# Optimization experiments

Measured on AMD Instinct MI355X. Metric: run time of the kernel, lower is better.

Reference implementation:

```python
import jax, jax.numpy as jnp
import numpy as np

N_SAMPLES = 32768
WS, STEP = 2048, 256
DILATIONS = (1, 2, 4, 8, 16, 32, 64, 1)
N_KEEP = 16
N_ROOMS = 8
N_ATOMS = 2048


def stft_mag(x):
    # x: (B, 1, N) -> magnitude spectrogram (B, 128, 1025)
    B = x.shape[0]
    xx = jnp.pad(x.reshape(B, -1), ((0, 0), (0, WS - STEP)))  # right-pad -> exactly N/STEP frames
    n_frames = N_SAMPLES // STEP  # 128
    idx = jnp.arange(n_frames)[:, None] * STEP + jnp.arange(WS)[None, :]
    frames = xx[:, idx] * jnp.hanning(WS)[None, None, :]  # (B, 128, 2048)
    return jnp.abs(jnp.fft.rfft(frames, axis=-1))


def fft_convolve(a, b):
    # linear convolution via zero-padding to 2N, sliced back to N
    n = a.shape[-1]
    pad = [(0, 0)] * (a.ndim - 1) + [(0, n)]
    sa = jnp.fft.rfft(jnp.pad(a, pad), axis=-1)
    sb = jnp.fft.rfft(jnp.pad(b, pad), axis=-1)
    return jnp.fft.irfft(sa * sb, n=2 * n, axis=-1)[..., :n]


def mlp(z, w, b, g, be, ow, ob):
    # LinearOutputStack: (Linear -> LayerNorm -> leaky_relu) x3 -> Linear
    for i in range(w.shape[0]):
        z = z @ w[i] + b[i]
        mu = jnp.mean(z, -1, keepdims=True)
        var = jnp.var(z, -1, keepdims=True)
        z = (z - mu) / jnp.sqrt(var + 1e-5) * g[i] + be[i]
        z = jax.nn.leaky_relu(z, 0.2)
    return z @ ow + ob


def setup_inputs() -> dict:
    key = jax.random.key(0)
    ks = jax.random.split(key, 12)
    s = 0.02
    B = 4
    decay = jnp.linspace(1.0, 0.0, N_SAMPLES) ** 2
    atoms = jax.random.uniform(ks[0], (N_ATOMS, N_SAMPLES), minval=-0.01, maxval=0.01) * decay[None, :]
    imp = jax.random.normal(ks[1], (N_ROOMS, N_SAMPLES)) * (jnp.linspace(1.0, 0.0, N_SAMPLES) ** 4)[None, :]
    imp = imp / jnp.linalg.norm(imp, axis=-1, keepdims=True)
    return {
        'x': jax.random.normal(ks[2], (B, 1, N_SAMPLES)),
        'atoms': atoms,
        'enc_w': jax.random.normal(ks[3], (8, 1024, 1024, 2)) * s,
        'enc_b': jnp.zeros((8, 1024)),
        'up_w': jax.random.normal(ks[4], (256, 1024)) * s,
        'up_b': jnp.zeros((256,)),
        'lat_w': jax.random.normal(ks[5], (1024, 16)) * s,
        'lat_b': jnp.zeros((16,)),
        'room_w': jax.random.normal(ks[6], (3, 16, 16)) * s,
        'room_b': jnp.zeros((3, 16)),
        'room_g': jnp.ones((3, 16)),
        'room_be': jnp.zeros((3, 16)),
        'room_ow': jax.random.normal(ks[7], (16, N_ROOMS)) * s,
        'room_ob': jnp.zeros((N_ROOMS,)),
        'mix_w': jax.random.normal(ks[8], (3, 16, 16)) * s,
        'mix_b': jnp.zeros((3, 16)),
        'mix_g': jnp.ones((3, 16)),
        'mix_be': jnp.zeros((3, 16)),
        'mix_ow': jax.random.normal(ks[9], (16, 1)) * s,
        'mix_ob': jnp.zeros((1,)),
        'impulses': imp,
    }


def reference(x, atoms, enc_w, enc_b, up_w, up_b, lat_w, lat_b,
              room_w, room_b, room_g, room_be, room_ow, room_ob,
              mix_w, mix_b, mix_g, mix_be, mix_ow, mix_ob, impulses):
    B = x.shape[0]
    # ---- encode ----
    spec = stft_mag(x)[..., :1024]                    # (B, 128, 1024)
    h = jnp.transpose(spec, (0, 2, 1))                # (B, 1024, 128)
    for i, d in enumerate(DILATIONS):                  # anti-causal dilated residual stack
        y = jnp.pad(h, ((0, 0), (0, 0), (0, d)))      # pad the FUTURE
        y = jax.lax.conv_general_dilated(y, enc_w[i], (1,), 'VALID', rhs_dilation=(d,),
                                         dimension_numbers=('NCH', 'OIH', 'NCH'))
        h = h + jax.nn.leaky_relu(y + enc_b[i][None, :, None], 0.2)
    z = jnp.mean(h, axis=-1)                          # (B, 1024)
    dense = z @ lat_w + lat_b                          # (B, 16)
    dense = dense / (jnp.linalg.norm(dense, axis=-1, keepdims=True) + 1e-8)  # unit_norm
    # ---- generate ----
    enc = jnp.einsum('bct,oc->bot', h, up_w) + up_b[None, :, None]  # 1x1 conv -> (B, 256, 128)
    full = jnp.zeros((B, 256, N_SAMPLES), enc.dtype).at[:, :, ::STEP].set(enc)
    # sparsify2: flattened top-k over (channel, time)
    flat = full.reshape(B, -1)
    vals, idx = jax.lax.top_k(flat, N_KEEP)           # (B, 16)
    ch = idx // N_SAMPLES                              # atom/channel index per event
    t = idx % N_SAMPLES                                # time index per event
    packed = jnp.zeros((B, N_KEEP, N_SAMPLES), full.dtype).at[
        jnp.arange(B)[:, None], jnp.arange(N_KEEP)[None, :], t].set(vals)
    subset = atoms[ch]                                 # gather -> (B, 16, 32768)
    events = fft_convolve(packed, subset)              # (B, 16, N)
    dry = jnp.sum(events, axis=1, keepdims=True)       # (B, 1, N)
    # ---- reverb ----
    room = jax.nn.softmax(mlp(dense, room_w, room_b, room_g, room_be, room_ow, room_ob), axis=-1)
    impulse = room @ impulses                          # (B, N)
    wet = fft_convolve(dry, impulse[:, None, :])
    mix = jax.nn.sigmoid(mlp(dense, mix_w, mix_b, mix_g, mix_be, mix_ow, mix_ob))[:, :, None]  # (B,1,1)
    return dry * mix + wet * (1.0 - mix)
```

## Files before the change

### kernel.cpp

```cpp
#include <hip/hip_runtime.h>
#include <hip/hip_bf16.h>
#include <math.h>

#define NSMP 32768
#define NFR 128
#define NCH 1024
#define NB 4

typedef __attribute__((ext_vector_type(8))) short short8;
typedef __attribute__((ext_vector_type(4))) float f32x4;
typedef unsigned short ushort;

__device__ __forceinline__ void split_bf(float v, ushort& h, ushort& l) {
  __hip_bfloat16 bh = __float2bfloat16(v);
  float r = v - __bfloat162float(bh);
  __hip_bfloat16 bl = __float2bfloat16(r);
  h = *reinterpret_cast<ushort*>(&bh);
  l = *reinterpret_cast<ushort*>(&bl);
}

__device__ __forceinline__ void gload_lds16(const ushort* g, ushort* l) {
  __builtin_amdgcn_global_load_lds((const __attribute__((address_space(1))) void*)g,
                                   (__attribute__((address_space(3))) void*)l, 16, 0, 0);
}

__global__ __launch_bounds__(256) void stft_kernel(const float* __restrict__ x,
                                                   float* __restrict__ h,
                                                   ushort* __restrict__ hTh,
                                                   ushort* __restrict__ hTl) {
  __shared__ float re[2048];
  __shared__ float im[2048];
  __shared__ float twr[1024];
  __shared__ float twi[1024];
  int bid = blockIdx.x;
  int b = bid >> 7;
  int f = bid & 127;
  int tid = threadIdx.x;
  const float TWO_PI = 6.28318530717958647692f;
  for (int k = tid; k < 1024; k += 256) {
    float ang = -TWO_PI * (float)k / 2048.0f;
    float sn, cs;
    sincosf(ang, &sn, &cs);
    twr[k] = cs; twi[k] = sn;
  }
  for (int i = tid; i < 2048; i += 256) {
    int rev = (int)(__brev((unsigned)i) >> 21);
    int pos = f * 256 + rev;
    float v = (pos < NSMP) ? x[b * NSMP + pos] : 0.f;
    float w = 0.5f - 0.5f * cosf(TWO_PI * (float)rev / 2047.0f);
    re[i] = v * w;
    im[i] = 0.f;
  }
  __syncthreads();
  for (int s = 0; s < 11; ++s) {
    for (int q = 0; q < 4; ++q) {
      int bi = tid + q * 256;
      int half = 1 << s;
      int j = bi & (half - 1);
      int i0 = ((bi >> s) << (s + 1)) | j;
      int i1 = i0 + half;
      int ti = j << (10 - s);
      float cs = twr[ti], sn = twi[ti];
      float ur = re[i0], ui = im[i0];
      float vr = re[i1], vi = im[i1];
      float tr = vr * cs - vi * sn;
      float tti = vr * sn + vi * cs;
      re[i0] = ur + tr; im[i0] = ui + tti;
      re[i1] = ur - tr; im[i1] = ui - tti;
    }
    __syncthreads();
  }
  for (int k = tid; k < 1024; k += 256) {
    float m = sqrtf(re[k] * re[k] + im[k] * im[k]);
    h[(b * NCH + k) * NFR + f] = m;
    ushort hi, lo;
    split_bf(m, hi, lo);
    size_t tidx = ((size_t)b * 192 + f) * 1024 + k;
    hTh[tidx] = hi;
    hTl[tidx] = lo;
  }
}

__global__ void zeropad_kernel(ushort* p0, ushort* p1, ushort* p2, ushort* p3) {
  int row = 128 + blockIdx.x;
  int b = blockIdx.y;
  size_t idx = ((size_t)b * 192 + row) * 1024 + threadIdx.x * 4;
  uint2 z = {0u, 0u};
  *(uint2*)&p0[idx] = z;
  *(uint2*)&p1[idx] = z;
  *(uint2*)&p2[idx] = z;
  *(uint2*)&p3[idx] = z;
}

__global__ __launch_bounds__(256) void wsplit_kernel(const float* __restrict__ encw,
                                                     ushort* __restrict__ w0h, ushort* __restrict__ w0l,
                                                     ushort* __restrict__ w1h, ushort* __restrict__ w1l) {
  size_t F = (size_t)blockIdx.x * 256 + threadIdx.x;
  float4 v = ((const float4*)encw)[F];
  size_t lo_idx = F >> 9;
  int c0 = (int)(F & 511) * 2;
  size_t base = lo_idx * 1024 + c0;
  ushort h0, l0, h1, l1;
  split_bf(v.x, h0, l0);
  split_bf(v.z, h1, l1);
  *(ushort2*)&w0h[base] = (ushort2){h0, h1};
  *(ushort2*)&w0l[base] = (ushort2){l0, l1};
  split_bf(v.y, h0, l0);
  split_bf(v.w, h1, l1);
  *(ushort2*)&w1h[base] = (ushort2){h0, h1};
  *(ushort2*)&w1l[base] = (ushort2){l0, l1};
}

__global__ __launch_bounds__(256) void conv_mfma(const ushort* __restrict__ hTh,
                                                 const ushort* __restrict__ hTl,
                                                 const ushort* __restrict__ w0h, const ushort* __restrict__ w0l,
                                                 const ushort* __restrict__ w1h, const ushort* __restrict__ w1l,
                                                 int D, float* __restrict__ yp) {
  __shared__ ushort lds[24576];
  int tid = threadIdx.x;
  int og = blockIdx.x * 64;
  int b = blockIdx.y;
  int s = blockIdx.z;
  int wid = tid >> 6, lane = tid & 63;
  int wr = (wid >> 1) * 32, wc = (wid & 1) * 64;
  int lr = lane & 15, lk = lane >> 4;
  int srow = lane >> 2;
  int scol = ((lane & 3) ^ ((lane >> 3) & 3)) * 8;

  f32x4 acc[2][4];
#pragma unroll
  for (int m = 0; m < 2; ++m)
#pragma unroll
    for (int n = 0; n < 4; ++n) acc[m][n] = (f32x4){0.f, 0.f, 0.f, 0.f};

  const ushort* hb_h = hTh + (size_t)b * 192 * 1024;
  const ushort* hb_l = hTl + (size_t)b * 192 * 1024;

  auto stage = [&](int buf, int p) {
    const ushort* Wh = (p < 4) ? w0h : w1h;
    const ushort* Wl = (p < 4) ? w0l : w1l;
    int rowoff = (p < 4) ? 0 : D;
    int c0 = s * 128 + (p & 3) * 32 + scol;
    ushort* base = &lds[buf * 12288];
    int ra = og + wid * 16 + srow;
    gload_lds16(Wh + (size_t)ra * 1024 + c0, base + wid * 512);
    gload_lds16(Wl + (size_t)ra * 1024 + c0, base + 2048 + wid * 512);
    int rb0 = rowoff + wid * 32 + srow;
    int rb1 = rb0 + 16;
    gload_lds16(hb_h + (size_t)rb0 * 1024 + c0, base + 4096 + wid * 1024);
    gload_lds16(hb_h + (size_t)rb1 * 1024 + c0, base + 4096 + wid * 1024 + 512);
    gload_lds16(hb_l + (size_t)rb0 * 1024 + c0, base + 8192 + wid * 1024);
    gload_lds16(hb_l + (size_t)rb1 * 1024 + c0, base + 8192 + wid * 1024 + 512);
  };

  auto compute = [&](int buf) {
    const ushort* base = &lds[buf * 12288];
    short8 ah[2], al[2], bh[4], bl[4];
#pragma unroll
    for (int m = 0; m < 2; ++m) {
      int ar = wr + m * 16 + lr;
      int off = ar * 32 + ((lk ^ ((ar >> 1) & 3)) << 3);
      ah[m] = *(const short8*)&base[off];
      al[m] = *(const short8*)&base[2048 + off];
    }
#pragma unroll
    for (int n = 0; n < 4; ++n) {
      int br = wc + n * 16 + lr;
      int off = br * 32 + ((lk ^ ((br >> 1) & 3)) << 3);
      bh[n] = *(const short8*)&base[4096 + off];
      bl[n] = *(const short8*)&base[8192 + off];
    }
#pragma unroll
    for (int m = 0; m < 2; ++m)
#pragma unroll
      for (int n = 0; n < 4; ++n) {
        acc[m][n] = __builtin_amdgcn_mfma_f32_16x16x32_bf16(ah[m], bh[n], acc[m][n], 0, 0, 0);
        acc[m][n] = __builtin_amdgcn_mfma_f32_16x16x32_bf16(ah[m], bl[n], acc[m][n], 0, 0, 0);
        acc[m][n] = __builtin_amdgcn_mfma_f32_16x16x32_bf16(al[m], bh[n], acc[m][n], 0, 0, 0);
      }
  };

  stage(0, 0);
  asm volatile("s_waitcnt vmcnt(0)" ::: "memory");
  __syncthreads();
#pragma unroll 2
  for (int p = 0; p < 8; ++p) {
    if (p < 7) stage((p + 1) & 1, p + 1);
    compute(p & 1);
    asm volatile("s_waitcnt vmcnt(0)" ::: "memory");
    __syncthreads();
  }

  float* dst = yp + (size_t)(s * 4 + b) * 131072;
#pragma unroll
  for (int m = 0; m < 2; ++m)
#pragma unroll
    for (int n = 0; n < 4; ++n)
#pragma unroll
      for (int r = 0; r < 4; ++r) {
        int orow = og + wr + m * 16 + lk * 4 + r;
        int col = wc + n * 16 + lr;
        dst[orow * 128 + col] = acc[m][n][r];
      }
}

__global__ __launch_bounds__(256) void conv_epi(const float* __restrict__ yp,
                                                const float* __restrict__ hin,
                                                const float* __restrict__ bias,
                                                float* __restrict__ hout,
                                                ushort* __restrict__ hTh,
                                                ushort* __restrict__ hTl) {
  __shared__ float T[16][132];
  int og = blockIdx.x * 16;
  int b = blockIdx.y;
  int tid = threadIdx.x;
#pragma unroll
  for (int j = 0; j < 8; ++j) {
    int flat = j * 256 + tid;
    int o = flat >> 7, t = flat & 127;
    size_t base = ((size_t)b * NCH + og + o) * NFR + t;
    float v = 0.f;
#pragma unroll
    for (int sl = 0; sl < 8; ++sl) v += yp[(size_t)sl * 524288 + base];
    v += bias[og + o];
    v = (v > 0.f) ? v : 0.2f * v;
    float r = hin[base] + v;
    hout[base] = r;
    T[o][t] = r;
  }
  __syncthreads();
#pragma unroll
  for (int j = 0; j < 8; ++j) {
    int flat = j * 256 + tid;
    int t = flat >> 4, o = flat & 15;
    ushort hi, lo;
    split_bf(T[o][t], hi, lo);
    size_t tidx = ((size_t)b * 192 + t) * 1024 + og + o;
    hTh[tidx] = hi;
    hTl[tidx] = lo;
  }
}

template <int TAPS, int D, int KTOT, int SPLIT, int MROWS>
__global__ __launch_bounds__(256, 2) void gemm_f32(const float* __restrict__ hin,
                                                   const float* __restrict__ W,
                                                   float* __restrict__ yp) {
  __shared__ float As[64][68];
  __shared__ float Bs[64][132];
  int tid = threadIdx.x;
  int og = blockIdx.x * 64;
  int b = blockIdx.y;
  int s = blockIdx.z;
  const float* hb = hin + (size_t)b * (NCH * NFR);
  int tx = tid & 15;
  int ty = tid >> 4;
  float acc[4][8] = {};
  const int KS = KTOT / SPLIT;
  for (int kt = 0; kt < KS / 64; ++kt) {
    int k0 = s * KS + kt * 64;
    __syncthreads();
    {
      int r = tid >> 2;
      int seg = (tid & 3) * 16;
      const float4* src = (const float4*)(W + (size_t)(og + r) * KTOT + k0 + seg);
#pragma unroll
      for (int q = 0; q < 4; ++q) {
        float4 v = src[q];
        int row = seg + 4 * q;
#pragma unroll
        for (int i = 0; i < 4; ++i) {
          int rr = row + i;
          int col = r ^ (((rr >> 4) & 1) << 2);
          float val = (i == 0) ? v.x : (i == 1) ? v.y : (i == 2) ? v.z : v.w;
          As[rr][col] = val;
        }
      }
    }
    {
      int r = tid >> 2;
      int tq = (tid & 3) * 32;
      int c = k0 + r;
      const float4* src = (const float4*)(hb + (size_t)c * NFR + tq);
#pragma unroll
      for (int q = 0; q < 8; ++q) *(float4*)&Bs[r][tq + 4 * q] = src[q];
    }
    __syncthreads();
#pragma unroll 8
    for (int kk = 0; kk < 64; ++kk) {
      int ca = (ty * 4) ^ (((kk >> 4) & 1) << 2);
      float4 a0 = *(const float4*)&As[kk][ca];
      float4 b0 = *(const float4*)&Bs[kk][tx * 4];
      float4 b1 = *(const float4*)&Bs[kk][tx * 4 + 64];
      float av[4] = {a0.x, a0.y, a0.z, a0.w};
      float bv[8] = {b0.x, b0.y, b0.z, b0.w, b1.x, b1.y, b1.z, b1.w};
#pragma unroll
      for (int i = 0; i < 4; ++i)
#pragma unroll
        for (int j = 0; j < 8; ++j)
          acc[i][j] += av[i] * bv[j];
    }
  }
  float* ypb = yp + (size_t)s * (NB * MROWS * NFR) + (size_t)b * MROWS * NFR;
#pragma unroll
  for (int i = 0; i < 4; ++i) {
    int o = og + ty * 4 + i;
    *(float4*)&ypb[o * NFR + tx * 4] = (float4){acc[i][0], acc[i][1], acc[i][2], acc[i][3]};
    *(float4*)&ypb[o * NFR + tx * 4 + 64] = (float4){acc[i][4], acc[i][5], acc[i][6], acc[i][7]};
  }
}

__global__ __launch_bounds__(256) void dense_mlp_kernel(
    const float* __restrict__ h,
    const float* __restrict__ latw, const float* __restrict__ latb,
    const float* __restrict__ rw, const float* __restrict__ rb,
    const float* __restrict__ rg, const float* __restrict__ rbe,
    const float* __restrict__ rowt, const float* __restrict__ rob,
    const float* __restrict__ mw, const float* __restrict__ mb,
    const float* __restrict__ mg, const float* __restrict__ mbe,
    const float* __restrict__ mow, const float* __restrict__ mob,
    float* __restrict__ room, float* __restrict__ mixv) {
  __shared__ float z[1024];
  int b = blockIdx.x;
  int tid = threadIdx.x;
  const float* hb = h + b * NCH * NFR;
  for (int c = tid; c < 1024; c += 256) {
    float s = 0.f;
    const float* r = hb + c * NFR;
#pragma unroll 8
    for (int t = 0; t < NFR; ++t) s += r[t];
    z[c] = s * (1.f / 128.f);
  }
  __syncthreads();
  if (tid >= 64) return;
  int j = tid & 15;
  int p = tid >> 4;
  float dsum = 0.f;
  for (int c = p * 256; c < p * 256 + 256; ++c)
    dsum += z[c] * latw[c * 16 + j];
  dsum += __shfl_xor(dsum, 16);
  dsum += __shfl_xor(dsum, 32);
  float dj = dsum + latb[j];
  float sq = dj * dj;
  sq += __shfl_xor(sq, 1, 16);
  sq += __shfl_xor(sq, 2, 16);
  sq += __shfl_xor(sq, 4, 16);
  sq += __shfl_xor(sq, 8, 16);
  float a = dj / (sqrtf(sq) + 1e-8f);

  const float* W = rw;  const float* Bb = rb;
  const float* G = rg;  const float* Be = rbe;
  for (int which = 0; which < 2; ++which) {
    float v = a;
    for (int l = 0; l < 3; ++l) {
      float accv = Bb[l * 16 + j];
      for (int k = 0; k < 16; ++k) {
        float ak = __shfl(v, (tid & 48) | k);
        accv += ak * W[(l * 16 + k) * 16 + j];
      }
      float mu = accv;
      mu += __shfl_xor(mu, 1, 16); mu += __shfl_xor(mu, 2, 16);
      mu += __shfl_xor(mu, 4, 16); mu += __shfl_xor(mu, 8, 16);
      mu *= (1.f / 16.f);
      float dv = accv - mu;
      float var = dv * dv;
      var += __shfl_xor(var, 1, 16); var += __shfl_xor(var, 2, 16);
      var += __shfl_xor(var, 4, 16); var += __shfl_xor(var, 8, 16);
      var *= (1.f / 16.f);
      float xn = dv * rsqrtf(var + 1e-5f) * G[l * 16 + j] + Be[l * 16 + j];
      v = (xn > 0.f) ? xn : 0.2f * xn;
    }
    if (which == 0) {
      int r = tid & 7;
      float logit = rob[r];
      for (int k = 0; k < 16; ++k) {
        float ak = __shfl(v, (tid & 48) | k);
        logit += ak * rowt[k * 8 + r];
      }
      float mx = logit;
      mx = fmaxf(mx, __shfl_xor(mx, 1, 8));
      mx = fmaxf(mx, __shfl_xor(mx, 2, 8));
      mx = fmaxf(mx, __shfl_xor(mx, 4, 8));
      float e = expf(logit - mx);
      float se = e;
      se += __shfl_xor(se, 1, 8);
      se += __shfl_xor(se, 2, 8);
      se += __shfl_xor(se, 4, 8);
      if (tid < 8) room[b * 8 + r] = e / se;
      W = mw; Bb = mb; G = mg; Be = mbe;
    } else {
      float logit = mob[0];
      for (int k = 0; k < 16; ++k) {
        float ak = __shfl(v, (tid & 48) | k);
        logit += ak * mow[k];
      }
      if (tid == 0) mixv[b] = 1.f / (1.f + expf(-logit));
    }
  }
}

__global__ __launch_bounds__(256) void topk_kernel(const float* __restrict__ ep,
                                                   const float* __restrict__ upb,
                                                   float* __restrict__ vals,
                                                   int* __restrict__ chs,
                                                   int* __restrict__ tps) {
  __shared__ float swv[4];
  __shared__ int swi[4];
  int b = blockIdx.x;
  int tid = threadIdx.x;
  const float* e = ep + b * 32768;
  float lv[16];
  int li[16];
#pragma unroll
  for (int q = 0; q < 16; ++q) { lv[q] = -INFINITY; li[q] = 0x7fffffff; }
  for (int i = tid; i < 32768; i += 256) {
    float v = e[i] + e[131072 + i] + e[262144 + i] + e[393216 + i] + upb[i >> 7];
    if (v > lv[15]) {
      float cv = v; int ci = i;
#pragma unroll
      for (int q = 0; q < 16; ++q) {
        if (cv > lv[q]) {
          float tv = lv[q]; int ti = li[q];
          lv[q] = cv; li[q] = ci;
          cv = tv; ci = ti;
        }
      }
    }
  }
  for (int round = 0; round < 16; ++round) {
    float cv = lv[0];
    int ci = li[0];
#pragma unroll
    for (int off = 1; off < 64; off <<= 1) {
      float ov = __shfl_xor(cv, off);
      int oi = __shfl_xor(ci, off);
      if (ov > cv || (ov == cv && oi < ci)) { cv = ov; ci = oi; }
    }
    if ((tid & 63) == 0) { swv[tid >> 6] = cv; swi[tid >> 6] = ci; }
    __syncthreads();
    float wv = swv[0]; int wi = swi[0];
#pragma unroll
    for (int w = 1; w < 4; ++w) {
      float v2 = swv[w]; int i2 = swi[w];
      if (v2 > wv || (v2 == wv && i2 < wi)) { wv = v2; wi = i2; }
    }
    if (tid == 0) {
      vals[b * 16 + round] = (wv > 0.f) ? wv : 0.f;
      chs[b * 16 + round] = wi >> 7;
      tps[b * 16 + round] = (wi & 127) * 256;
    }
    if (li[0] == wi) {
#pragma unroll
      for (int q = 0; q < 15; ++q) { lv[q] = lv[q + 1]; li[q] = li[q + 1]; }
      lv[15] = -INFINITY; li[15] = 0x7fffffff;
    }
    __syncthreads();
  }
}

__global__ void dry_kernel(const float* __restrict__ atoms,
                           const float* __restrict__ vals, const int* __restrict__ chs,
                           const int* __restrict__ tps, float* __restrict__ dry) {
  int b = blockIdx.y;
  int n = blockIdx.x * 256 + threadIdx.x;
  float acc = 0.f;
#pragma unroll 4
  for (int j = 0; j < 16; ++j) {
    float v = vals[b * 16 + j];
    int tp = tps[b * 16 + j];
    int ch = chs[b * 16 + j];
    if (v != 0.f && n >= tp)
      acc += v * atoms[(size_t)ch * NSMP + (n - tp)];
  }
  dry[b * NSMP + n] = acc;
}

__global__ void impulse_kernel(const float* __restrict__ imps,
                               const float* __restrict__ room, float* __restrict__ imp) {
  int b = blockIdx.y;
  int n = blockIdx.x * 256 + threadIdx.x;
  float acc = 0.f;
#pragma unroll
  for (int r = 0; r < 8; ++r)
    acc += room[b * 8 + r] * imps[r * NSMP + n];
  imp[b * NSMP + n] = acc;
}

#define IS(a) is[(a) + ((a) >> 5)]
__global__ __launch_bounds__(256) void wet_kernel(const float* __restrict__ dry,
                                                  const float* __restrict__ impulse,
                                                  float* __restrict__ wp) {
  int s = blockIdx.x;
  int nt = blockIdx.y;
  int b = blockIdx.z;
  if (s > nt) return;
  __shared__ float is[4224];
  __shared__ float dsr[2048];
  int tid = threadIdx.x;
  int n0 = nt * 2048;
  int m0 = s * 2048;
  int base = n0 - m0 - 2047;
  const float* impb = impulse + b * NSMP;
  for (int k = tid; k < 4096; k += 256) {
    int idx = base + k;
    IS(k) = (idx >= 0 && idx < NSMP) ? impb[idx] : 0.f;
  }
  for (int i = tid; i < 2048; i += 256)
    dsr[i] = dry[b * NSMP + m0 + 2047 - i];
  __syncthreads();
  int aw = tid * 8;
  float w[8];
#pragma unroll
  for (int j = 0; j < 8; ++j) w[j] = IS(aw + j);
  float acc[8] = {};
  for (int jb = 0; jb < 2048; jb += 8) {
    float4 d0 = *(const float4*)&dsr[jb];
    float4 d1 = *(const float4*)&dsr[jb + 4];
    float dv[8] = {d0.x, d0.y, d0.z, d0.w, d1.x, d1.y, d1.z, d1.w};
#pragma unroll
    for (int e = 0; e < 8; ++e) {
      float dval = dv[e];
#pragma unroll
      for (int i = 0; i < 8; ++i)
        acc[i] += dval * w[(e + i) & 7];
      w[e] = IS(aw + jb + e + 8);
    }
  }
  float* dst = wp + (size_t)s * (NB * NSMP) + (size_t)b * NSMP + n0 + aw;
  *(float4*)dst = (float4){acc[0], acc[1], acc[2], acc[3]};
  *(float4*)(dst + 4) = (float4){acc[4], acc[5], acc[6], acc[7]};
}

__global__ void out_kernel(const float* __restrict__ dry, const float* __restrict__ wp,
                           const float* __restrict__ mixv, float* __restrict__ out) {
  int b = blockIdx.y;
  int n = blockIdx.x * 256 + threadIdx.x;
  float m = mixv[b];
  float wv = 0.f;
  int smax = n >> 11;
  for (int s = 0; s <= smax; ++s)
    wv += wp[(size_t)s * (NB * NSMP) + b * NSMP + n];
  out[b * NSMP + n] = dry[b * NSMP + n] * m + wv * (1.f - m);
}

extern "C" void kernel_launch(void* const* d_in, const int* in_sizes, int n_in,
                              void* d_out, int out_size, void* d_ws, size_t ws_size,
                              hipStream_t stream) {
  const float* x    = (const float*)d_in[0];
  const float* atoms= (const float*)d_in[1];
  const float* encw = (const float*)d_in[2];
  const float* encb = (const float*)d_in[3];
  const float* upw  = (const float*)d_in[4];
  const float* upb  = (const float*)d_in[5];
  const float* latw = (const float*)d_in[6];
  const float* latb = (const float*)d_in[7];
  const float* rw   = (const float*)d_in[8];
  const float* rb   = (const float*)d_in[9];
  const float* rg   = (const float*)d_in[10];
  const float* rbe  = (const float*)d_in[11];
  const float* rowt = (const float*)d_in[12];
  const float* rob  = (const float*)d_in[13];
  const float* mw   = (const float*)d_in[14];
  const float* mb   = (const float*)d_in[15];
  const float* mg   = (const float*)d_in[16];
  const float* mbe  = (const float*)d_in[17];
  const float* mow  = (const float*)d_in[18];
  const float* mob  = (const float*)d_in[19];
  const float* imps = (const float*)d_in[20];

  float* f    = (float*)d_ws;
  float* h0   = f;
  float* h1   = f + 524288;
  float* yp   = f + 1048576;
  float* ep   = yp;
  float* wp   = yp + 524288;
  float* dry  = f + 5242880;
  float* imp  = f + 5373952;
  float* room = f + 5636096;
  float* mixv = f + 5636128;
  float* vals = f + 5636160;
  int*   chs  = (int*)(f + 5636224);
  int*   tps  = (int*)(f + 5636288);
  ushort* w0h  = (ushort*)(f + 6000000);
  ushort* w0l  = w0h + 8388608;
  ushort* w1h  = w0l + 8388608;
  ushort* w1l  = w1h + 8388608;
  ushort* hTh0 = w1l + 8388608;
  ushort* hTl0 = hTh0 + 786432;
  ushort* hTh1 = hTl0 + 786432;
  ushort* hTl1 = hTh1 + 786432;

  wsplit_kernel<<<16384, 256, 0, stream>>>(encw, w0h, w0l, w1h, w1l);
  zeropad_kernel<<<dim3(64, 4), 256, 0, stream>>>(hTh0, hTl0, hTh1, hTl1);
  stft_kernel<<<512, 256, 0, stream>>>(x, h0, hTh0, hTl0);

  float* bufs[2] = {h0, h1};
  ushort* hThb[2] = {hTh0, hTh1};
  ushort* hTlb[2] = {hTl0, hTl1};
  const int dil[8] = {1, 2, 4, 8, 16, 32, 64, 1};
  for (int l = 0; l < 8; ++l) {
    int pi = l & 1, po = (l + 1) & 1;
    conv_mfma<<<dim3(16, 4, 8), 256, 0, stream>>>(
        hThb[pi], hTlb[pi],
        w0h + (size_t)l * 1048576, w0l + (size_t)l * 1048576,
        w1h + (size_t)l * 1048576, w1l + (size_t)l * 1048576,
        dil[l], yp);
    conv_epi<<<dim3(64, 4), 256, 0, stream>>>(yp, bufs[pi], encb + l * 1024,
                                              bufs[po], hThb[po], hTlb[po]);
  }

  dense_mlp_kernel<<<4, 256, 0, stream>>>(h0, latw, latb, rw, rb, rg, rbe, rowt, rob,
                                          mw, mb, mg, mbe, mow, mob, room, mixv);
  gemm_f32<1, 0, 1024, 4, 256><<<dim3(4, 4, 4), 256, 0, stream>>>(h0, upw, ep);
  topk_kernel<<<4, 256, 0, stream>>>(ep, upb, vals, chs, tps);
  dry_kernel<<<dim3(128, 4), 256, 0, stream>>>(atoms, vals, chs, tps, dry);
  impulse_kernel<<<dim3(128, 4), 256, 0, stream>>>(imps, room, imp);
  wet_kernel<<<dim3(16, 16, 4), 256, 0, stream>>>(dry, imp, wp);
  out_kernel<<<dim3(128, 4), 256, 0, stream>>>(dry, wp, mixv, (float*)d_out);
}
```

Measured before the change: 522.7 us.

## Enlarge conv MFMA tile, triple-buffer staging, fuse small kernels, split gemm K

The dilated-conv MFMA kernel now computes a 128x128 output tile per block instead of 64x128. It uses three LDS buffers with a prefetch depth of two, and each wave loads one operand plane. The zero-pad kernel is folded into the STFT kernel, and the dry and impulse kernels are merged into one launch. The up-projection gemm is split over 16 K-slices, which topk sums. These changes aim to raise data reuse and cut launch overhead, at the cost of fewer conv blocks (less parallelism), more LDS per block and more partial-sum traffic.

```diff
diff --git a/kernel.cpp b/kernel.cpp
--- a/kernel.cpp
+++ b/kernel.cpp
@@ -27,7 +27,9 @@
 __global__ __launch_bounds__(256) void stft_kernel(const float* __restrict__ x,
                                                    float* __restrict__ h,
                                                    ushort* __restrict__ hTh,
-                                                   ushort* __restrict__ hTl) {
+                                                   ushort* __restrict__ hTl,
+                                                   ushort* __restrict__ hTh1,
+                                                   ushort* __restrict__ hTl1) {
   __shared__ float re[2048];
   __shared__ float im[2048];
   __shared__ float twr[1024];
@@ -37,6 +39,12 @@
   int f = bid & 127;
   int tid = threadIdx.x;
   const float TWO_PI = 6.28318530717958647692f;
+  if (f < 64) {
+    size_t pidx = ((size_t)b * 192 + 128 + f) * 1024 + tid * 4;
+    uint2 z = {0u, 0u};
+    *(uint2*)&hTh[pidx] = z;  *(uint2*)&hTl[pidx] = z;
+    *(uint2*)&hTh1[pidx] = z; *(uint2*)&hTl1[pidx] = z;
+  }
   for (int k = tid; k < 1024; k += 256) {
     float ang = -TWO_PI * (float)k / 2048.0f;
     float sn, cs;
@@ -79,17 +87,6 @@
     hTh[tidx] = hi;
     hTl[tidx] = lo;
   }
-}
-
-__global__ void zeropad_kernel(ushort* p0, ushort* p1, ushort* p2, ushort* p3) {
-  int row = 128 + blockIdx.x;
-  int b = blockIdx.y;
-  size_t idx = ((size_t)b * 192 + row) * 1024 + threadIdx.x * 4;
-  uint2 z = {0u, 0u};
-  *(uint2*)&p0[idx] = z;
-  *(uint2*)&p1[idx] = z;
-  *(uint2*)&p2[idx] = z;
-  *(uint2*)&p3[idx] = z;
 }
 
 __global__ __launch_bounds__(256) void wsplit_kernel(const float* __restrict__ encw,
@@ -116,20 +113,20 @@
                                                  const ushort* __restrict__ w0h, const ushort* __restrict__ w0l,
                                                  const ushort* __restrict__ w1h, const ushort* __restrict__ w1l,
                                                  int D, float* __restrict__ yp) {
-  __shared__ ushort lds[24576];
+  __shared__ ushort lds[49152];
   int tid = threadIdx.x;
-  int og = blockIdx.x * 64;
+  int og = blockIdx.x * 128;
   int b = blockIdx.y;
   int s = blockIdx.z;
   int wid = tid >> 6, lane = tid & 63;
-  int wr = (wid >> 1) * 32, wc = (wid & 1) * 64;
+  int wr = (wid >> 1) * 64, wc = (wid & 1) * 64;
   int lr = lane & 15, lk = lane >> 4;
   int srow = lane >> 2;
-  int scol = ((lane & 3) ^ ((lane >> 3) & 3)) * 8;
-
-  f32x4 acc[2][4];
-#pragma unroll
-  for (int m = 0; m < 2; ++m)
+  int sgr = ((lane & 3) ^ ((lane >> 3) & 3)) * 8;
+
+  f32x4 acc[4][4];
+#pragma unroll
+  for (int m = 0; m < 4; ++m)
 #pragma unroll
     for (int n = 0; n < 4; ++n) acc[m][n] = (f32x4){0.f, 0.f, 0.f, 0.f};
 
@@ -140,38 +137,39 @@
     const ushort* Wh = (p < 4) ? w0h : w1h;
     const ushort* Wl = (p < 4) ? w0l : w1l;
     int rowoff = (p < 4) ? 0 : D;
-    int c0 = s * 128 + (p & 3) * 32 + scol;
-    ushort* base = &lds[buf * 12288];
-    int ra = og + wid * 16 + srow;
-    gload_lds16(Wh + (size_t)ra * 1024 + c0, base + wid * 512);
-    gload_lds16(Wl + (size_t)ra * 1024 + c0, base + 2048 + wid * 512);
-    int rb0 = rowoff + wid * 32 + srow;
-    int rb1 = rb0 + 16;
-    gload_lds16(hb_h + (size_t)rb0 * 1024 + c0, base + 4096 + wid * 1024);
-    gload_lds16(hb_h + (size_t)rb1 * 1024 + c0, base + 4096 + wid * 1024 + 512);
-    gload_lds16(hb_l + (size_t)rb0 * 1024 + c0, base + 8192 + wid * 1024);
-    gload_lds16(hb_l + (size_t)rb1 * 1024 + c0, base + 8192 + wid * 1024 + 512);
+    int c0 = s * 128 + (p & 3) * 32 + sgr;
+    ushort* dbase = &lds[buf * 16384 + wid * 4096];
+#pragma unroll
+    for (int j = 0; j < 8; ++j) {
+      int row = j * 16 + srow;
+      const ushort* src;
+      if (wid == 0)      src = Wh   + (size_t)(og + row) * 1024 + c0;
+      else if (wid == 1) src = Wl   + (size_t)(og + row) * 1024 + c0;
+      else if (wid == 2) src = hb_h + (size_t)(rowoff + row) * 1024 + c0;
+      else               src = hb_l + (size_t)(rowoff + row) * 1024 + c0;
+      gload_lds16(src, dbase + j * 512);
+    }
   };
 
   auto compute = [&](int buf) {
-    const ushort* base = &lds[buf * 12288];
-    short8 ah[2], al[2], bh[4], bl[4];
-#pragma unroll
-    for (int m = 0; m < 2; ++m) {
+    const ushort* base = &lds[buf * 16384];
+    short8 ah[4], al[4], bh[4], bl[4];
+#pragma unroll
+    for (int m = 0; m < 4; ++m) {
       int ar = wr + m * 16 + lr;
       int off = ar * 32 + ((lk ^ ((ar >> 1) & 3)) << 3);
       ah[m] = *(const short8*)&base[off];
-      al[m] = *(const short8*)&base[2048 + off];
+      al[m] = *(const short8*)&base[4096 + off];
     }
 #pragma unroll
     for (int n = 0; n < 4; ++n) {
       int br = wc + n * 16 + lr;
       int off = br * 32 + ((lk ^ ((br >> 1) & 3)) << 3);
-      bh[n] = *(const short8*)&base[4096 + off];
-      bl[n] = *(const short8*)&base[8192 + off];
-    }
-#pragma unroll
-    for (int m = 0; m < 2; ++m)
+      bh[n] = *(const short8*)&base[8192 + off];
+      bl[n] = *(const short8*)&base[12288 + off];
+    }
+#pragma unroll
+    for (int m = 0; m < 4; ++m)
 #pragma unroll
       for (int n = 0; n < 4; ++n) {
         acc[m][n] = __builtin_amdgcn_mfma_f32_16x16x32_bf16(ah[m], bh[n], acc[m][n], 0, 0, 0);
@@ -181,19 +179,19 @@
   };
 
   stage(0, 0);
-  asm volatile("s_waitcnt vmcnt(0)" ::: "memory");
-  __syncthreads();
-#pragma unroll 2
+  stage(1, 1);
+#pragma unroll
   for (int p = 0; p < 8; ++p) {
-    if (p < 7) stage((p + 1) & 1, p + 1);
-    compute(p & 1);
-    asm volatile("s_waitcnt vmcnt(0)" ::: "memory");
-    __syncthreads();
+    if (p < 7) asm volatile("s_waitcnt vmcnt(8)" ::: "memory");
+    else       asm volatile("s_waitcnt vmcnt(0)" ::: "memory");
+    __builtin_amdgcn_s_barrier();
+    if (p + 2 < 8) stage((p + 2) % 3, p + 2);
+    compute(p % 3);
   }
 
   float* dst = yp + (size_t)(s * 4 + b) * 131072;
 #pragma unroll
-  for (int m = 0; m < 2; ++m)
+  for (int m = 0; m < 4; ++m)
 #pragma unroll
     for (int n = 0; n < 4; ++n)
 #pragma unroll
@@ -413,7 +411,9 @@
 #pragma unroll
   for (int q = 0; q < 16; ++q) { lv[q] = -INFINITY; li[q] = 0x7fffffff; }
   for (int i = tid; i < 32768; i += 256) {
-    float v = e[i] + e[131072 + i] + e[262144 + i] + e[393216 + i] + upb[i >> 7];
+    float v = upb[i >> 7];
+#pragma unroll
+    for (int sl = 0; sl < 16; ++sl) v += e[(size_t)sl * 131072 + i];
     if (v > lv[15]) {
       float cv = v; int ci = i;
 #pragma unroll
@@ -457,9 +457,11 @@
   }
 }
 
-__global__ void dry_kernel(const float* __restrict__ atoms,
-                           const float* __restrict__ vals, const int* __restrict__ chs,
-                           const int* __restrict__ tps, float* __restrict__ dry) {
+__global__ void dryimp_kernel(const float* __restrict__ atoms,
+                              const float* __restrict__ vals, const int* __restrict__ chs,
+                              const int* __restrict__ tps, const float* __restrict__ imps,
+                              const float* __restrict__ room,
+                              float* __restrict__ dry, float* __restrict__ imp) {
   int b = blockIdx.y;
   int n = blockIdx.x * 256 + threadIdx.x;
   float acc = 0.f;
@@ -472,17 +474,11 @@
       acc += v * atoms[(size_t)ch * NSMP + (n - tp)];
   }
   dry[b * NSMP + n] = acc;
-}
-
-__global__ void impulse_kernel(const float* __restrict__ imps,
-                               const float* __restrict__ room, float* __restrict__ imp) {
-  int b = blockIdx.y;
-  int n = blockIdx.x * 256 + threadIdx.x;
-  float acc = 0.f;
+  float ia = 0.f;
 #pragma unroll
   for (int r = 0; r < 8; ++r)
-    acc += room[b * 8 + r] * imps[r * NSMP + n];
-  imp[b * NSMP + n] = acc;
+    ia += room[b * 8 + r] * imps[r * NSMP + n];
+  imp[b * NSMP + n] = ia;
 }
 
 #define IS(a) is[(a) + ((a) >> 5)]
@@ -590,8 +586,7 @@
   ushort* hTl1 = hTh1 + 786432;
 
   wsplit_kernel<<<16384, 256, 0, stream>>>(encw, w0h, w0l, w1h, w1l);
-  zeropad_kernel<<<dim3(64, 4), 256, 0, stream>>>(hTh0, hTl0, hTh1, hTl1);
-  stft_kernel<<<512, 256, 0, stream>>>(x, h0, hTh0, hTl0);
+  stft_kernel<<<512, 256, 0, stream>>>(x, h0, hTh0, hTl0, hTh1, hTl1);
 
   float* bufs[2] = {h0, h1};
   ushort* hThb[2] = {hTh0, hTh1};
@@ -599,7 +594,7 @@
   const int dil[8] = {1, 2, 4, 8, 16, 32, 64, 1};
   for (int l = 0; l < 8; ++l) {
     int pi = l & 1, po = (l + 1) & 1;
-    conv_mfma<<<dim3(16, 4, 8), 256, 0, stream>>>(
+    conv_mfma<<<dim3(8, 4, 8), 256, 0, stream>>>(
         hThb[pi], hTlb[pi],
         w0h + (size_t)l * 1048576, w0l + (size_t)l * 1048576,
         w1h + (size_t)l * 1048576, w1l + (size_t)l * 1048576,
@@ -610,10 +605,9 @@
 
   dense_mlp_kernel<<<4, 256, 0, stream>>>(h0, latw, latb, rw, rb, rg, rbe, rowt, rob,
                                           mw, mb, mg, mbe, mow, mob, room, mixv);
-  gemm_f32<1, 0, 1024, 4, 256><<<dim3(4, 4, 4), 256, 0, stream>>>(h0, upw, ep);
+  gemm_f32<1, 0, 1024, 16, 256><<<dim3(4, 4, 16), 256, 0, stream>>>(h0, upw, ep);
   topk_kernel<<<4, 256, 0, stream>>>(ep, upb, vals, chs, tps);
-  dry_kernel<<<dim3(128, 4), 256, 0, stream>>>(atoms, vals, chs, tps, dry);
-  impulse_kernel<<<dim3(128, 4), 256, 0, stream>>>(imps, room, imp);
+  dryimp_kernel<<<dim3(128, 4), 256, 0, stream>>>(atoms, vals, chs, tps, imps, room, dry, imp);
   wet_kernel<<<dim3(16, 16, 4), 256, 0, stream>>>(dry, imp, wp);
   out_kernel<<<dim3(128, 4), 256, 0, stream>>>(dry, wp, mixv, (float*)d_out);
 }
```

After: 532.8 us. About the same (+1.9%).
